# Optimization experiments

Measured on AMD Instinct MI355X. Metric: run time of the kernel, lower is better.

Reference implementation:

```python
import math
import jax, jax.numpy as jnp
import numpy as np

B, S, D, K = 64, 512, 4096, 8
COND_H, SIG_F, SIG_H = 256, 128, 256


def setup_inputs() -> dict:
    key = jax.random.key(0)
    ks = jax.random.split(key, 12)
    emb = jax.random.normal(ks[0], (B, S, D), dtype=jnp.float32)
    seqlens = jax.random.randint(ks[1], (B,), 0, S - K, dtype=jnp.int64)
    timesteps = jax.random.uniform(ks[2], (B,), dtype=jnp.float32)
    # cond_mlp: Linear(D, COND_H) -> GELU -> Linear(COND_H, K*D)
    W1 = jax.random.normal(ks[3], (D, COND_H), dtype=jnp.float32) / np.sqrt(D)
    b1 = jax.random.normal(ks[4], (COND_H,), dtype=jnp.float32) * 0.01
    W2 = jax.random.normal(ks[5], (COND_H, K * D), dtype=jnp.float32) / np.sqrt(COND_H)
    b2 = jax.random.normal(ks[6], (K * D,), dtype=jnp.float32) * 0.01
    # sigma_mlp: Linear(SIG_F, SIG_H) -> SiLU -> Linear(SIG_H, K*D)
    sW1 = jax.random.normal(ks[7], (SIG_F, SIG_H), dtype=jnp.float32) / np.sqrt(SIG_F)
    sb1 = jax.random.normal(ks[8], (SIG_H,), dtype=jnp.float32) * 0.01
    sW2 = jax.random.normal(ks[9], (SIG_H, K * D), dtype=jnp.float32) / np.sqrt(SIG_H)
    sb2 = jax.random.normal(ks[10], (K * D,), dtype=jnp.float32) * 0.01
    return {"crossattn_emb": emb, "crossattn_seqlens": seqlens, "timesteps": timesteps,
            "W1": W1, "b1": b1, "W2": W2, "b2": b2,
            "sW1": sW1, "sb1": sb1, "sW2": sW2, "sb2": sb2}


def _sigma_features(t):
    # sinusoidal features over sigma, dim SIG_F (half cos, half sin)
    half = SIG_F // 2
    freqs = jnp.exp(-math.log(10000.0) * jnp.arange(half, dtype=jnp.float32) / half)
    ang = t.astype(jnp.float32)[:, None] * freqs[None, :]  # [B, half]
    return jnp.concatenate([jnp.cos(ang), jnp.sin(ang)], axis=-1)  # [B, SIG_F]


def reference(crossattn_emb, crossattn_seqlens, timesteps,
              W1, b1, W2, b2, sW1, sb1, sW2, sb2):
    b, s, d = crossattn_emb.shape
    # masked mean-pool over content slots
    pos = jnp.arange(s)[None, :]
    mask = (pos < crossattn_seqlens[:, None]).astype(crossattn_emb.dtype)  # [B,S]
    denom = jnp.clip(jnp.sum(mask, axis=1, keepdims=True), 1.0)
    pooled = jnp.einsum('bsd,bs->bd', crossattn_emb, mask) / denom  # [B,D]
    # cond MLP (exact GELU, matching torch nn.GELU default)
    h = jax.nn.gelu(pooled @ W1 + b1, approximate=False)
    postfix = (h @ W2 + b2).reshape(b, K, d)
    # sigma-conditional residual
    sh = jax.nn.silu(_sigma_features(timesteps) @ sW1 + sb1)
    postfix = postfix + (sh @ sW2 + sb2).reshape(b, K, d)
    # front_of_padding splice: overwrite [seqlen, seqlen+K) per sample
    offsets = crossattn_seqlens[:, None] + jnp.arange(K)[None, :]  # [B,K]
    return crossattn_emb.at[jnp.arange(b)[:, None], offsets].set(postfix)
```

## Files before the change

kernel.cpp:

```cpp
#include <hip/hip_runtime.h>
#include <math.h>

#define BB 64
#define SS 512
#define DD 4096
#define KK 8
#define COND_H 256
#define SIG_F 128
#define SIG_H 256
#define KD (KK*DD)
#define SCHUNKS 8
#define SROWS (SS/SCHUNKS)
#define KSLICES 64
#define KSL (DD/KSLICES)
#define PADC 260

typedef float f32x4 __attribute__((ext_vector_type(4)));
__device__ inline f32x4 nt_load4(const float* p) {
    return __builtin_nontemporal_load((const f32x4*)p);
}
__device__ inline void nt_store4(float* p, f32x4 v) {
    __builtin_nontemporal_store(v, (f32x4*)p);
}

__device__ inline bool seql_is64(const int* sq) {
    bool is64 = true;
#pragma unroll
    for (int i = 1; i < 64; i += 2) is64 &= (sq[i] == 0);
    return is64;
}
__device__ inline int load_seqlen(const int* sq, int b, bool is64) {
    return is64 ? sq[2 * b] : sq[b];
}

__global__ __launch_bounds__(256) void k_copy_pool(
        const float* __restrict__ emb, const int* __restrict__ seql_raw,
        float* __restrict__ out, float* __restrict__ partial) {
    const int dchunk = blockIdx.x;
    const int sy     = blockIdx.y;
    const int b      = blockIdx.z;
    const int tid    = threadIdx.x;
    const int d0     = dchunk * 1024 + tid * 4;

    const bool is64 = seql_is64(seql_raw);
    const int  sl   = load_seqlen(seql_raw, b, is64);

    size_t base = ((size_t)b * SS + (size_t)sy * SROWS) * DD + d0;
    f32x4 sum = {0.f, 0.f, 0.f, 0.f};

    const int s0 = sy * SROWS;
#pragma unroll 4
    for (int i = 0; i < SROWS; ++i) {
        f32x4 v = nt_load4(emb + base);
        nt_store4(out + base, v);
        if (s0 + i < sl) sum += v;
        base += DD;
    }
    size_t pidx = ((size_t)sy * BB + b) * DD + d0;
    *(f32x4*)(partial + pidx) = sum;
}

__global__ __launch_bounds__(256) void k_l1_split(
        const float* __restrict__ partial, const int* __restrict__ seql_raw,
        const float* __restrict__ W1, const float* __restrict__ tsteps,
        const float* __restrict__ sW1, const float* __restrict__ sb1,
        float* __restrict__ ph, float* __restrict__ sh_ws) {
    __shared__ float smem[8][SIG_F];
    const int tid = threadIdx.x;

    if (blockIdx.x < 512) {
        const int ks = blockIdx.x >> 3;
        const int bg = blockIdx.x & 7;
        const bool is64 = seql_is64(seql_raw);

#pragma unroll
        for (int e = 0; e < 2; ++e) {
            int idx = e * 256 + tid;
            int b8  = idx >> 6;
            int d   = idx & (KSL - 1);
            int b   = bg * 8 + b8;
            float s = 0.f;
            size_t col = (size_t)ks * KSL + d;
#pragma unroll
            for (int sy = 0; sy < SCHUNKS; ++sy)
                s += partial[((size_t)sy * BB + b) * DD + col];
            float denom = fmaxf((float)load_seqlen(seql_raw, b, is64), 1.0f);
            smem[b8][d] = s / denom;
        }
        __syncthreads();

        float acc[8];
#pragma unroll
        for (int i = 0; i < 8; ++i) acc[i] = 0.f;
#pragma unroll 8
        for (int k = 0; k < KSL; ++k) {
            float w = W1[((size_t)ks * KSL + k) * COND_H + tid];
#pragma unroll
            for (int b8 = 0; b8 < 8; ++b8)
                acc[b8] = fmaf(smem[b8][k], w, acc[b8]);
        }
#pragma unroll
        for (int b8 = 0; b8 < 8; ++b8)
            ph[((size_t)ks * BB + bg * 8 + b8) * COND_H + tid] = acc[b8];
    } else {
        const int sb = blockIdx.x - 512;
#pragma unroll
        for (int e = 0; e < 4; ++e) {
            int idx = e * 256 + tid;
            int b8  = idx >> 7;
            int f   = idx & 127;
            float t = tsteps[sb * 8 + b8];
            int fi = (f < 64) ? f : (f - 64);
            float fr = expf(-0.14391156831213413f * (float)fi);
            float ang = t * fr;
            smem[b8][f] = (f < 64) ? cosf(ang) : sinf(ang);
        }
        __syncthreads();

        float acc[8];
#pragma unroll
        for (int i = 0; i < 8; ++i) acc[i] = sb1[tid];
#pragma unroll 8
        for (int c = 0; c < SIG_F; ++c) {
            float w = sW1[c * SIG_H + tid];
#pragma unroll
            for (int b8 = 0; b8 < 8; ++b8)
                acc[b8] = fmaf(smem[b8][c], w, acc[b8]);
        }
#pragma unroll
        for (int b8 = 0; b8 < 8; ++b8) {
            float a = acc[b8];
            float s = a / (1.0f + expf(-a));
            sh_ws[(sb * 8 + b8) * SIG_H + tid] = s;
        }
    }
}

__global__ __launch_bounds__(256) void k_l1_finish(
        const float* __restrict__ ph, const float* __restrict__ b1,
        float* __restrict__ h_ws) {
    const int b = blockIdx.x;
    const int tid = threadIdx.x;
    float acc = b1[tid];
#pragma unroll 8
    for (int ks = 0; ks < KSLICES; ++ks)
        acc += ph[((size_t)ks * BB + b) * COND_H + tid];
    float g = 0.5f * acc * (1.0f + erff(acc * 0.70710678118654752f));
    h_ws[b * COND_H + tid] = g;
}

__global__ __launch_bounds__(256) void k_layer2_splice(
        const float* __restrict__ h_ws, const float* __restrict__ sh_ws,
        const float* __restrict__ W2, const float* __restrict__ b2,
        const float* __restrict__ sW2, const float* __restrict__ sb2,
        const int* __restrict__ seql_raw, float* __restrict__ out) {
    __shared__ float hl[BB][PADC];
    __shared__ float sl_[BB][PADC];
    const int tid = threadIdx.x;
    const int tj  = tid & 15;
    const int bg  = tid >> 4;
    const int j   = blockIdx.x * 64 + tj * 4;

#pragma unroll
    for (int e = 0; e < 16; ++e) {
        int idx = e * 256 + tid;
        int row = idx >> 6;
        int c4i = idx & 63;
        *(float4*)&hl[row][c4i * 4]  = *(const float4*)&h_ws[row * COND_H + c4i * 4];
        *(float4*)&sl_[row][c4i * 4] = *(const float4*)&sh_ws[row * COND_H + c4i * 4];
    }
    __syncthreads();

    float acc[4][4];
#pragma unroll
    for (int i = 0; i < 4; ++i)
#pragma unroll
        for (int q = 0; q < 4; ++q) acc[i][q] = 0.0f;

    for (int pass = 0; pass < 2; ++pass) {
        const float* __restrict__ Wm = pass ? sW2 : W2;
        const float (*A)[PADC] = pass ? sl_ : hl;
#pragma unroll 2
        for (int c4 = 0; c4 < COND_H / 4; ++c4) {
            float wf[4][4];
#pragma unroll
            for (int cc = 0; cc < 4; ++cc) {
                float4 w = *(const float4*)&Wm[(size_t)(c4 * 4 + cc) * KD + j];
                wf[cc][0] = w.x; wf[cc][1] = w.y; wf[cc][2] = w.z; wf[cc][3] = w.w;
            }
#pragma unroll
            for (int b4 = 0; b4 < 4; ++b4) {
                const float4 av = *(const float4*)&A[bg * 4 + b4][c4 * 4];
#pragma unroll
                for (int jj = 0; jj < 4; ++jj) {
                    float a = acc[b4][jj];
                    a = fmaf(av.x, wf[0][jj], a);
                    a = fmaf(av.y, wf[1][jj], a);
                    a = fmaf(av.z, wf[2][jj], a);
                    a = fmaf(av.w, wf[3][jj], a);
                    acc[b4][jj] = a;
                }
            }
        }
    }

    float4 bb = *(const float4*)&b2[j];
    float4 sb = *(const float4*)&sb2[j];
    bb.x += sb.x; bb.y += sb.y; bb.z += sb.z; bb.w += sb.w;

    const int k = j >> 12;
    const int d = j & (DD - 1);
    const bool is64 = seql_is64(seql_raw);
#pragma unroll
    for (int b4 = 0; b4 < 4; ++b4) {
        const int b = bg * 4 + b4;
        const int sl = load_seqlen(seql_raw, b, is64);
        size_t o = ((size_t)b * SS + (size_t)(sl + k)) * DD + d;
        float4 v;
        v.x = acc[b4][0] + bb.x;
        v.y = acc[b4][1] + bb.y;
        v.z = acc[b4][2] + bb.z;
        v.w = acc[b4][3] + bb.w;
        *(float4*)&out[o] = v;
    }
}

extern "C" void kernel_launch(void* const* d_in, const int* in_sizes, int n_in,
                              void* d_out, int out_size, void* d_ws, size_t ws_size,
                              hipStream_t stream) {
    const float* emb    = (const float*)d_in[0];
    const int*   seql   = (const int*)  d_in[1];
    const float* tsteps = (const float*)d_in[2];
    const float* W1     = (const float*)d_in[3];
    const float* b1     = (const float*)d_in[4];
    const float* W2     = (const float*)d_in[5];
    const float* b2     = (const float*)d_in[6];
    const float* sW1    = (const float*)d_in[7];
    const float* sb1    = (const float*)d_in[8];
    const float* sW2    = (const float*)d_in[9];
    const float* sb2    = (const float*)d_in[10];
    float* out = (float*)d_out;

    const size_t PART_FLOATS = (size_t)SCHUNKS * BB * DD;
    const size_t PH_FLOATS   = (size_t)KSLICES * BB * COND_H;
    float* partial = (float*)d_ws;
    float* ph      = partial + PART_FLOATS;
    float* h_ws    = ph + PH_FLOATS;
    float* sh_ws   = h_ws + (size_t)BB * COND_H;

    hipLaunchKernelGGL(k_copy_pool, dim3(4, 8, 64), dim3(256), 0, stream,
                       emb, seql, out, partial);
    hipLaunchKernelGGL(k_l1_split, dim3(520), dim3(256), 0, stream,
                       partial, seql, W1, tsteps, sW1, sb1, ph, sh_ws);
    hipLaunchKernelGGL(k_l1_finish, dim3(64), dim3(256), 0, stream,
                       ph, b1, h_ws);
    hipLaunchKernelGGL(k_layer2_splice, dim3(512), dim3(256), 0, stream,
                       h_ws, sh_ws, W2, b2, sW2, sb2, seql, out);
}
```

Baseline: 263.9 us.

## Drop nontemporal copy, widen copy rows per block, remove LDS staging in layer2

```diff
diff --git a/kernel.cpp b/kernel.cpp
--- a/kernel.cpp
+++ b/kernel.cpp
@@ -13,15 +13,8 @@
 #define SROWS (SS/SCHUNKS)
 #define KSLICES 64
 #define KSL (DD/KSLICES)
-#define PADC 260
 
 typedef float f32x4 __attribute__((ext_vector_type(4)));
-__device__ inline f32x4 nt_load4(const float* p) {
-    return __builtin_nontemporal_load((const f32x4*)p);
-}
-__device__ inline void nt_store4(float* p, f32x4 v) {
-    __builtin_nontemporal_store(v, (f32x4*)p);
-}
 
 __device__ inline bool seql_is64(const int* sq) {
     bool is64 = true;
@@ -36,28 +29,38 @@
 __global__ __launch_bounds__(256) void k_copy_pool(
         const float* __restrict__ emb, const int* __restrict__ seql_raw,
         float* __restrict__ out, float* __restrict__ partial) {
-    const int dchunk = blockIdx.x;
-    const int sy     = blockIdx.y;
-    const int b      = blockIdx.z;
-    const int tid    = threadIdx.x;
-    const int d0     = dchunk * 1024 + tid * 4;
+    const int sy  = blockIdx.x;
+    const int b   = blockIdx.y;
+    const int tid = threadIdx.x;
 
     const bool is64 = seql_is64(seql_raw);
     const int  sl   = load_seqlen(seql_raw, b, is64);
-
-    size_t base = ((size_t)b * SS + (size_t)sy * SROWS) * DD + d0;
-    f32x4 sum = {0.f, 0.f, 0.f, 0.f};
-
-    const int s0 = sy * SROWS;
-#pragma unroll 4
-    for (int i = 0; i < SROWS; ++i) {
-        f32x4 v = nt_load4(emb + base);
-        nt_store4(out + base, v);
-        if (s0 + i < sl) sum += v;
-        base += DD;
-    }
-    size_t pidx = ((size_t)sy * BB + b) * DD + d0;
-    *(f32x4*)(partial + pidx) = sum;
+    const int  s0   = sy * SROWS;
+
+    const float* __restrict__ src = emb + ((size_t)b * SS + s0) * DD;
+    float* __restrict__ dst       = out + ((size_t)b * SS + s0) * DD;
+
+    f32x4 sum[4];
+#pragma unroll
+    for (int c = 0; c < 4; ++c) sum[c] = (f32x4){0.f, 0.f, 0.f, 0.f};
+
+#pragma unroll 2
+    for (int r = 0; r < SROWS; ++r) {
+        const size_t ro = (size_t)r * DD;
+        const bool in = (s0 + r) < sl;
+#pragma unroll
+        for (int c = 0; c < 4; ++c) {
+            const size_t off = ro + (size_t)(c * 256 + tid) * 4;
+            f32x4 v = *(const f32x4*)(src + off);
+            *(f32x4*)(dst + off) = v;
+            if (in) sum[c] += v;
+        }
+    }
+
+    float* pp = partial + ((size_t)sy * BB + b) * DD;
+#pragma unroll
+    for (int c = 0; c < 4; ++c)
+        *(f32x4*)(pp + (size_t)(c * 256 + tid) * 4) = sum[c];
 }
 
 __global__ __launch_bounds__(256) void k_l1_split(
@@ -154,32 +157,20 @@
         const float* __restrict__ W2, const float* __restrict__ b2,
         const float* __restrict__ sW2, const float* __restrict__ sb2,
         const int* __restrict__ seql_raw, float* __restrict__ out) {
-    __shared__ float hl[BB][PADC];
-    __shared__ float sl_[BB][PADC];
-    const int tid = threadIdx.x;
-    const int tj  = tid & 15;
-    const int bg  = tid >> 4;
-    const int j   = blockIdx.x * 64 + tj * 4;
-
-#pragma unroll
-    for (int e = 0; e < 16; ++e) {
-        int idx = e * 256 + tid;
-        int row = idx >> 6;
-        int c4i = idx & 63;
-        *(float4*)&hl[row][c4i * 4]  = *(const float4*)&h_ws[row * COND_H + c4i * 4];
-        *(float4*)&sl_[row][c4i * 4] = *(const float4*)&sh_ws[row * COND_H + c4i * 4];
-    }
-    __syncthreads();
-
-    float acc[4][4];
-#pragma unroll
-    for (int i = 0; i < 4; ++i)
+    const int tid = threadIdx.x;
+    const int tj  = tid & 7;
+    const int bg  = tid >> 3;
+    const int j   = blockIdx.x * 32 + tj * 4;
+
+    float acc[2][4];
+#pragma unroll
+    for (int i = 0; i < 2; ++i)
 #pragma unroll
         for (int q = 0; q < 4; ++q) acc[i][q] = 0.0f;
 
     for (int pass = 0; pass < 2; ++pass) {
         const float* __restrict__ Wm = pass ? sW2 : W2;
-        const float (*A)[PADC] = pass ? sl_ : hl;
+        const float* __restrict__ Hs = pass ? sh_ws : h_ws;
 #pragma unroll 2
         for (int c4 = 0; c4 < COND_H / 4; ++c4) {
             float wf[4][4];
@@ -189,16 +180,16 @@
                 wf[cc][0] = w.x; wf[cc][1] = w.y; wf[cc][2] = w.z; wf[cc][3] = w.w;
             }
 #pragma unroll
-            for (int b4 = 0; b4 < 4; ++b4) {
-                const float4 av = *(const float4*)&A[bg * 4 + b4][c4 * 4];
+            for (int b2i = 0; b2i < 2; ++b2i) {
+                const float4 av = *(const float4*)&Hs[(bg * 2 + b2i) * COND_H + c4 * 4];
 #pragma unroll
                 for (int jj = 0; jj < 4; ++jj) {
-                    float a = acc[b4][jj];
+                    float a = acc[b2i][jj];
                     a = fmaf(av.x, wf[0][jj], a);
                     a = fmaf(av.y, wf[1][jj], a);
                     a = fmaf(av.z, wf[2][jj], a);
                     a = fmaf(av.w, wf[3][jj], a);
-                    acc[b4][jj] = a;
+                    acc[b2i][jj] = a;
                 }
             }
         }
@@ -212,15 +203,15 @@
     const int d = j & (DD - 1);
     const bool is64 = seql_is64(seql_raw);
 #pragma unroll
-    for (int b4 = 0; b4 < 4; ++b4) {
-        const int b = bg * 4 + b4;
+    for (int b2i = 0; b2i < 2; ++b2i) {
+        const int b = bg * 2 + b2i;
         const int sl = load_seqlen(seql_raw, b, is64);
         size_t o = ((size_t)b * SS + (size_t)(sl + k)) * DD + d;
         float4 v;
-        v.x = acc[b4][0] + bb.x;
-        v.y = acc[b4][1] + bb.y;
-        v.z = acc[b4][2] + bb.z;
-        v.w = acc[b4][3] + bb.w;
+        v.x = acc[b2i][0] + bb.x;
+        v.y = acc[b2i][1] + bb.y;
+        v.z = acc[b2i][2] + bb.z;
+        v.w = acc[b2i][3] + bb.w;
         *(float4*)&out[o] = v;
     }
 }
@@ -248,12 +239,12 @@
     float* h_ws    = ph + PH_FLOATS;
     float* sh_ws   = h_ws + (size_t)BB * COND_H;
 
-    hipLaunchKernelGGL(k_copy_pool, dim3(4, 8, 64), dim3(256), 0, stream,
+    hipLaunchKernelGGL(k_copy_pool, dim3(8, 64), dim3(256), 0, stream,
                        emb, seql, out, partial);
     hipLaunchKernelGGL(k_l1_split, dim3(520), dim3(256), 0, stream,
                        partial, seql, W1, tsteps, sW1, sb1, ph, sh_ws);
     hipLaunchKernelGGL(k_l1_finish, dim3(64), dim3(256), 0, stream,
                        ph, b1, h_ws);
-    hipLaunchKernelGGL(k_layer2_splice, dim3(512), dim3(256), 0, stream,
+    hipLaunchKernelGGL(k_layer2_splice, dim3(1024), dim3(256), 0, stream,
                        h_ws, sh_ws, W2, b2, sW2, sb2, seql, out);
 }
```

Result: slower. 348.3 us (+32.0%).
